# Performance work log

Hardware: AMD Instinct MI355X
Metric: run time of the kernel (lower is better)

## Reference

```python
import jax, jax.numpy as jnp
import numpy as np

D_MODEL = 768
D_STATE = 16
D_CONV = 4
EXPAND = 2
D_INNER = D_MODEL * EXPAND
B, L = 2, 2048


def _silu(x):
    return x * jax.nn.sigmoid(x)


def _ssm_core(xn, inw, cw, cb, xw, dtw, dtb, Alog, Dp, outw):
    """Mamba selective SSM. xn: [B,L,d_model] -> [B,L,d_model]."""
    Bn, Ln, _ = xn.shape
    S = Alog.shape[1]
    d_inner = Alog.shape[0]
    k = cw.shape[-1]
    xz = xn @ inw                      # [B,L,2*d_inner]
    xi, z = jnp.split(xz, 2, axis=-1)
    # depthwise causal conv along L (torch pads both sides then slices [:L] == left-pad k-1)
    xc = jnp.swapaxes(xi, 1, 2)        # [B,d_inner,L]
    xc = jax.lax.conv_general_dilated(xc, cw, (1,), [(k - 1, 0)],
                                      feature_group_count=d_inner)
    xc = xc + cb[None, :, None]
    xc = _silu(jnp.swapaxes(xc, 1, 2))  # [B,L,d_inner]
    bcdt = xc @ xw                     # [B,L,1+2S]
    dt_raw = bcdt[..., :1]
    Bs = bcdt[..., 1:1 + S]            # [B,L,S]
    Cs = bcdt[..., 1 + S:]             # [B,L,S]
    dt = jax.nn.softplus(dt_raw * dtw[None, None, :] + dtb)  # [B,L,d_inner]
    A = -jnp.exp(jnp.clip(Alog, -6.0, 6.0))                  # [d_inner,S]
    dA = jnp.exp(dt[..., None] * A[None, None])               # [B,L,d_inner,S]
    dBx = dt[..., None] * Bs[:, :, None, :] * xc[..., None]   # [B,L,d_inner,S]

    def step(h, ins):
        dA_t, dBx_t, C_t = ins
        h = jnp.clip(dA_t * h + dBx_t, -10000.0, 10000.0)
        return h, jnp.einsum('bds,bs->bd', h, C_t)

    h0 = jnp.zeros((Bn, d_inner, S), xc.dtype)
    _, ys = jax.lax.scan(step, h0, (jnp.moveaxis(dA, 1, 0),
                                    jnp.moveaxis(dBx, 1, 0),
                                    jnp.moveaxis(Cs, 1, 0)))
    y = jnp.moveaxis(ys, 0, 1) + xc * Dp[None, None]
    y = y * _silu(z)
    return y @ outw


def setup_inputs() -> dict:
    key = jax.random.key(0)
    ks = jax.random.split(key, 20)
    def core_params(koff):
        return dict(
            inw=jax.random.normal(ks[koff + 0], (D_MODEL, 2 * D_INNER), jnp.float32) * 0.02,
            cw=jax.random.normal(ks[koff + 1], (D_INNER, 1, D_CONV), jnp.float32) * 0.2,
            cb=jnp.zeros((D_INNER,), jnp.float32),
            xw=jax.random.normal(ks[koff + 2], (D_INNER, 1 + 2 * D_STATE), jnp.float32) * 0.02,
            dtw=jax.random.normal(ks[koff + 3], (D_INNER,), jnp.float32) * 0.5,
            dtb=jax.random.normal(ks[koff + 4], (D_INNER,), jnp.float32) * 0.1,
            Alog=jnp.clip(jnp.log(jnp.arange(1, D_STATE + 1, dtype=jnp.float32))[None, :]
                          * jnp.ones((D_INNER, 1), jnp.float32), -6.0, 6.0),
            D=jnp.ones((D_INNER,), jnp.float32),
            outw=jax.random.normal(ks[koff + 5], (D_INNER, D_MODEL), jnp.float32) * 0.02,
        )
    f = core_params(2)
    b = core_params(8)
    return {
        'x': jax.random.normal(ks[0], (B, L, D_MODEL), jnp.float32),
        'ln_g': jnp.ones((D_MODEL,), jnp.float32),
        'ln_b': jnp.zeros((D_MODEL,), jnp.float32),
        'alpha': jnp.zeros((), jnp.float32),
        'f_inw': f['inw'], 'f_cw': f['cw'], 'f_cb': f['cb'], 'f_xw': f['xw'],
        'f_dtw': f['dtw'], 'f_dtb': f['dtb'], 'f_Alog': f['Alog'], 'f_D': f['D'], 'f_outw': f['outw'],
        'b_inw': b['inw'], 'b_cw': b['cw'], 'b_cb': b['cb'], 'b_xw': b['xw'],
        'b_dtw': b['dtw'], 'b_dtb': b['dtb'], 'b_Alog': b['Alog'], 'b_D': b['D'], 'b_outw': b['outw'],
    }


def reference(x, ln_g, ln_b, alpha,
              f_inw, f_cw, f_cb, f_xw, f_dtw, f_dtb, f_Alog, f_D, f_outw,
              b_inw, b_cw, b_cb, b_xw, b_dtw, b_dtb, b_Alog, b_D, b_outw):
    residual = x.astype(jnp.float32)
    mu = residual.mean(-1, keepdims=True)
    var = ((residual - mu) ** 2).mean(-1, keepdims=True)
    xn = (residual - mu) / jnp.sqrt(var + 1e-5) * ln_g + ln_b
    y_fwd = _ssm_core(xn, f_inw, f_cw, f_cb, f_xw, f_dtw, f_dtb, f_Alog, f_D, f_outw)
    y_bwd = jnp.flip(_ssm_core(jnp.flip(xn, 1), b_inw, b_cw, b_cb, b_xw,
                               b_dtw, b_dtb, b_Alog, b_D, b_outw), 1)
    a = jax.nn.sigmoid(alpha)
    y = a * y_fwd + (1.0 - a) * y_bwd
    return y + residual
```

## Files before the change

kernel.cpp:

```cpp
#include <hip/hip_runtime.h>
#include <cstddef>
#include <cstdint>

#define DMODEL 768
#define DINNER 1536
#define NSTATE 16
#define LSEQ   2048
#define NB     2
#define NTOK   (NB*LSEQ)
#define NBCDT  33

#define TC     32
#define NCHUNK (LSEQ/TC)
#define KSPLIT 12
#define LOG2E  1.44269504f

typedef __bf16 bf16x8 __attribute__((ext_vector_type(8)));
typedef float  floatx4 __attribute__((ext_vector_type(4)));
typedef unsigned short us8 __attribute__((ext_vector_type(8)));

__device__ __forceinline__ float exp2_hw(float x) { return __builtin_amdgcn_exp2f(x); }
__device__ __forceinline__ float silu_f(float x) { return x / (1.f + expf(-x)); }
__device__ __forceinline__ float clip1e4(float x) {
    return __builtin_amdgcn_fmed3f(x, -1e4f, 1e4f);
}
__device__ __forceinline__ unsigned short f2bf(float f) {
    unsigned int u = __float_as_uint(f);
    unsigned int r = u + 0x7fffu + ((u >> 16) & 1u);
    return (unsigned short)(r >> 16);
}
__device__ __forceinline__ float bf2f(unsigned short u) {
    return __uint_as_float((unsigned int)u << 16);
}
__device__ __forceinline__ unsigned int pack2bf(float a, float b) {
    unsigned int ua = __float_as_uint(a); ua = ua + 0x7fffu + ((ua >> 16) & 1u);
    unsigned int ub = __float_as_uint(b); ub = ub + 0x7fffu + ((ub >> 16) & 1u);
    return (ua >> 16) | (ub & 0xffff0000u);
}
__device__ __forceinline__ void ld_lds16(unsigned short* lds, const unsigned short* g) {
    __builtin_amdgcn_global_load_lds(
        (const __attribute__((address_space(1))) unsigned int*)g,
        (__attribute__((address_space(3))) unsigned int*)lds,
        16, 0, 0);
}

__global__ void ln_kernel(const float* __restrict__ x,
                          const float* __restrict__ g,
                          const float* __restrict__ be,
                          unsigned short* __restrict__ xnb,
                          float* __restrict__ bcdt) {
    int row = blockIdx.x;
    int tid = threadIdx.x;
    int zi = row * 256 + tid;
    if (zi < 2 * NTOK * NBCDT) bcdt[zi] = 0.f;
    const float* xr = x + (size_t)row * DMODEL;
    float s = 0.f, ss = 0.f;
    for (int i = tid; i < DMODEL; i += 256) {
        float v = xr[i];
        s += v; ss += v * v;
    }
    for (int o = 32; o >= 1; o >>= 1) {
        s  += __shfl_xor(s,  o, 64);
        ss += __shfl_xor(ss, o, 64);
    }
    __shared__ float sS[4], sSS[4];
    int w = tid >> 6;
    if ((tid & 63) == 0) { sS[w] = s; sSS[w] = ss; }
    __syncthreads();
    s  = sS[0] + sS[1] + sS[2] + sS[3];
    ss = sSS[0] + sSS[1] + sSS[2] + sSS[3];
    float mu = s / DMODEL;
    float var = ss / DMODEL - mu * mu;
    float rstd = rsqrtf(var + 1e-5f);
    unsigned short* xo = xnb + (size_t)row * DMODEL;
    for (int i = tid; i < DMODEL; i += 256)
        xo[i] = f2bf((xr[i] - mu) * rstd * g[i] + be[i]);
}

__global__ __launch_bounds__(256)
void cast_weights(const float* __restrict__ f_inw, const float* __restrict__ b_inw,
                  const float* __restrict__ f_outw, const float* __restrict__ b_outw,
                  const float* __restrict__ f_xw, const float* __restrict__ b_xw,
                  const float* __restrict__ alpha,
                  unsigned short* __restrict__ inwT, unsigned short* __restrict__ outwT,
                  unsigned short* __restrict__ xwT) {
    __shared__ float t[32][33];
    int bid = blockIdx.x;
    int tid = threadIdx.x;
    int lr = tid >> 5, lc = tid & 31;
    if (bid < 4608) {
        int n0 = (bid % 192) * 32;
        int k0 = (bid / 192) * 32;
        const float* w = (n0 >= 3072) ? b_inw : f_inw;
        int nb = (n0 >= 3072) ? (n0 - 3072) : n0;
        #pragma unroll
        for (int r = 0; r < 4; r++)
            t[r * 8 + lr][lc] = w[(size_t)(k0 + r * 8 + lr) * 3072 + nb + lc];
        __syncthreads();
        #pragma unroll
        for (int r = 0; r < 4; r++)
            inwT[(size_t)(n0 + r * 8 + lr) * DMODEL + k0 + lc] = f2bf(t[lc][r * 8 + lr]);
    } else if (bid < 6912) {
        bid -= 4608;
        float a = 1.f / (1.f + expf(-alpha[0]));
        int n0 = (bid % 24) * 32;
        int k0 = (bid / 24) * 32;
        const float* w = (k0 >= DINNER) ? b_outw : f_outw;
        float sc = (k0 >= DINNER) ? (1.f - a) : a;
        int kb = (k0 >= DINNER) ? (k0 - DINNER) : k0;
        #pragma unroll
        for (int r = 0; r < 4; r++)
            t[r * 8 + lr][lc] = w[(size_t)(kb + r * 8 + lr) * DMODEL + n0 + lc];
        __syncthreads();
        #pragma unroll
        for (int r = 0; r < 4; r++)
            outwT[(size_t)(n0 + r * 8 + lr) * 3072 + k0 + lc] = f2bf(sc * t[lc][r * 8 + lr]);
    } else {
        bid -= 6912;
        int dir = bid / 48;
        int k0 = (bid % 48) * 32;
        const float* xw = dir ? b_xw : f_xw;
        unsigned short* dst = xwT + (size_t)dir * 48 * DINNER;
        for (int idx = tid; idx < 48 * 32; idx += 256) {
            int n = idx >> 5, kk = idx & 31;
            float v = (n < 33) ? xw[(size_t)(k0 + kk) * 33 + n] : 0.f;
            dst[(size_t)n * DINNER + k0 + kk] = f2bf(v);
        }
    }
}

__global__ __launch_bounds__(256)
void gemm_xz_mfma(const unsigned short* __restrict__ xnb,
                  const unsigned short* __restrict__ inwT,
                  unsigned short* __restrict__ xi, unsigned short* __restrict__ sz) {
    __shared__ unsigned short SH[128 * 136];
    unsigned short* Asm = SH;
    unsigned short* Bsm = SH + 128 * 64;
    int tid = threadIdx.x;
    int bm = blockIdx.y * 128;
    int bn = blockIdx.x * 128;
    int wave = tid >> 6, lane = tid & 63;
    int wm = (wave & 1) * 64, wn = (wave >> 1) * 64;
    int col15 = lane & 15, quad = lane >> 4;
    int lrow = lane >> 3;
    int lk   = (((lane & 7) ^ lrow) * 8);
    floatx4 acc[4][4];
    #pragma unroll
    for (int i = 0; i < 4; i++)
        #pragma unroll
        for (int j = 0; j < 4; j++)
            acc[i][j] = (floatx4){0.f, 0.f, 0.f, 0.f};

    int sw = col15 & 7;
    for (int k0 = 0; k0 < DMODEL; k0 += 64) {
        #pragma unroll
        for (int i = 0; i < 4; i++) {
            int r8 = wave * 32 + i * 8;
            int ra = r8 + lrow;
            ld_lds16(&Asm[r8 * 64], &xnb[(size_t)(bm + ra) * DMODEL + k0 + lk]);
            ld_lds16(&Bsm[r8 * 64], &inwT[(size_t)(bn + ra) * DMODEL + k0 + lk]);
        }
        __syncthreads();
        #pragma unroll
        for (int k2 = 0; k2 < 2; k2++) {
            bf16x8 af[4], bf_[4];
            int pc = ((k2 * 4 + quad) ^ sw) * 8;
            #pragma unroll
            for (int mt = 0; mt < 4; mt++)
                af[mt] = *(const bf16x8*)(&Asm[(wm + mt * 16 + col15) * 64 + pc]);
            #pragma unroll
            for (int nt = 0; nt < 4; nt++)
                bf_[nt] = *(const bf16x8*)(&Bsm[(wn + nt * 16 + col15) * 64 + pc]);
            #pragma unroll
            for (int mt = 0; mt < 4; mt++)
                #pragma unroll
                for (int nt = 0; nt < 4; nt++)
                    acc[mt][nt] = __builtin_amdgcn_mfma_f32_16x16x32_bf16(
                        af[mt], bf_[nt], acc[mt][nt], 0, 0, 0);
        }
        __syncthreads();
    }
    int dirq = (bn >= 3072) ? 1 : 0;
    int cb0  = bn - dirq * 3072;
    int zs   = (cb0 >= DINNER) ? 1 : 0;
    int ccb  = cb0 - zs * DINNER;
    unsigned short* dst = zs ? sz : xi;
    unsigned short* C16 = SH;
    #pragma unroll
    for (int mt = 0; mt < 4; mt++)
        #pragma unroll
        for (int nt = 0; nt < 4; nt++)
            #pragma unroll
            for (int r = 0; r < 4; r++) {
                int row = wm + mt * 16 + quad * 4 + r;
                int col = wn + nt * 16 + col15;
                float v = acc[mt][nt][r];
                if (zs) v = silu_f(v);
                C16[row * 136 + col] = f2bf(v);
            }
    __syncthreads();
    {
        int erow = tid >> 4;
        int cch  = tid & 15;
        size_t rowbase = (size_t)dirq * NTOK + bm;
        #pragma unroll
        for (int p = 0; p < 8; p++) {
            int row = p * 16 + erow;
            uint4 v = *(const uint4*)(&C16[row * 136 + cch * 8]);
            *(uint4*)(&dst[(rowbase + row) * DINNER + ccb + cch * 8]) = v;
        }
    }
}

__global__ __launch_bounds__(256)
void bcdt_conv_gemm_mfma(const unsigned short* __restrict__ xi,
                         const float* __restrict__ f_cw, const float* __restrict__ f_cb,
                         const float* __restrict__ b_cw, const float* __restrict__ b_cb,
                         const unsigned short* __restrict__ xwT,
                         float* __restrict__ bcdt) {
    __shared__ unsigned short Xs[131 * 64];
    __shared__ unsigned short As[128 * 64];
    __shared__ unsigned short Bs[48 * 64];
    int tid = threadIdx.x;
    int wave = tid >> 6, lane = tid & 63;
    int r0 = blockIdx.x * 128;
    int kc = blockIdx.y;
    int dirb = r0 >> 11;
    int dir = dirb >> 1, b = dirb & 1;
    int u0 = r0 & 2047;
    const float* cw = dir ? b_cw : f_cw;
    const float* cb = dir ? b_cb : f_cb;
    size_t xibase = ((size_t)dir * NTOK + (size_t)b * LSEQ) * DINNER;
    const unsigned short* Bsrc = xwT + (size_t)dir * 48 * DINNER;

    int col15 = lane & 15, quad = lane >> 4;
    int sw = col15 & 7;
    int lrow = lane >> 3;
    int lcc = (lane & 7) * 8;
    int lk  = (((lane & 7) ^ lrow) * 8);
    int wm = wave * 32;

    int cp = (tid & 31) * 2;
    int rg = (tid >> 5) * 16;

    floatx4 acc[2][3];
    #pragma unroll
    for (int i = 0; i < 2; i++)
        #pragma unroll
        for (int j = 0; j < 3; j++)
            acc[i][j] = (floatx4){0.f, 0.f, 0.f, 0.f};

    for (int ks = 0; ks < 2; ks++) {
        int kb = kc * 128 + ks * 64;
        #pragma unroll
        for (int i = 0; i < 2; i++) {
            int g = wave + i * 4;
            if (g < 6)
                ld_lds16(&Bs[g * 8 * 64],
                         &Bsrc[(size_t)(g * 8 + lrow) * DINNER + kb + lk]);
        }
        #pragma unroll
        for (int i = 0; i < 4; i++) {
            int g = wave * 4 + i;
            int u = u0 + g * 8 + lrow;
            int l = dir ? (LSEQ - 1 - u) : u;
            ld_lds16(&Xs[(3 + g * 8) * 64], &xi[xibase + (size_t)l * DINNER + kb + lcc]);
        }
        if (tid < 96) {
            int hh = tid >> 5, c2 = (tid & 31) * 2;
            int u = u0 - 3 + hh;
            unsigned int v = 0;
            if (u >= 0) {
                int l = dir ? (LSEQ - 1 - u) : u;
                v = *(const unsigned int*)(&xi[xibase + (size_t)l * DINNER + kb + c2]);
            }
            *(unsigned int*)(&Xs[hh * 64 + c2]) = v;
        }
        __syncthreads();
        {
            int ch0 = kb + cp;
            float4 w0 = *(const float4*)(cw + (size_t)ch0 * 4);
            float4 w1 = *(const float4*)(cw + (size_t)(ch0 + 1) * 4);
            float cb0 = cb[ch0], cb1 = cb[ch0 + 1];
            unsigned int v;
            v = *(const unsigned int*)(&Xs[(rg + 0) * 64 + cp]);
            float a3 = bf2f((unsigned short)v), b3 = bf2f((unsigned short)(v >> 16));
            v = *(const unsigned int*)(&Xs[(rg + 1) * 64 + cp]);
            float a2 = bf2f((unsigned short)v), b2 = bf2f((unsigned short)(v >> 16));
            v = *(const unsigned int*)(&Xs[(rg + 2) * 64 + cp]);
            float a1 = bf2f((unsigned short)v), b1 = bf2f((unsigned short)(v >> 16));
            int cs = cp >> 3, e = cp & 7;
            #pragma unroll
            for (int j = 0; j < 16; j++) {
                int r = rg + j;
                v = *(const unsigned int*)(&Xs[(r + 3) * 64 + cp]);
                float a0 = bf2f((unsigned short)v), b0 = bf2f((unsigned short)(v >> 16));
                float xa = cb0;
                xa = fmaf(w0.x, a3, xa); xa = fmaf(w0.y, a2, xa);
                xa = fmaf(w0.z, a1, xa); xa = fmaf(w0.w, a0, xa);
                xa = silu_f(xa);
                float xb = cb1;
                xb = fmaf(w1.x, b3, xb); xb = fmaf(w1.y, b2, xb);
                xb = fmaf(w1.z, b1, xb); xb = fmaf(w1.w, b0, xb);
                xb = silu_f(xb);
                a3 = a2; a2 = a1; a1 = a0;
                b3 = b2; b2 = b1; b1 = b0;
                int ad = r * 64 + ((cs ^ (r & 7)) << 3) + e;
                *(unsigned int*)(&As[ad]) = pack2bf(xa, xb);
            }
        }
        __syncthreads();
        #pragma unroll
        for (int k2 = 0; k2 < 2; k2++) {
            int pc = ((k2 * 4 + quad) ^ sw) * 8;
            bf16x8 af[2], bfr[3];
            #pragma unroll
            for (int mt = 0; mt < 2; mt++)
                af[mt] = *(const bf16x8*)(&As[(wm + mt * 16 + col15) * 64 + pc]);
            #pragma unroll
            for (int nt = 0; nt < 3; nt++)
                bfr[nt] = *(const bf16x8*)(&Bs[(nt * 16 + col15) * 64 + pc]);
            #pragma unroll
            for (int mt = 0; mt < 2; mt++)
                #pragma unroll
                for (int nt = 0; nt < 3; nt++)
                    acc[mt][nt] = __builtin_amdgcn_mfma_f32_16x16x32_bf16(
                        af[mt], bfr[nt], acc[mt][nt], 0, 0, 0);
        }
        __syncthreads();
    }
    #pragma unroll
    for (int mt = 0; mt < 2; mt++) {
        #pragma unroll
        for (int nt = 0; nt < 3; nt++) {
            int n = nt * 16 + col15;
            if (n < 33) {
                #pragma unroll
                for (int r = 0; r < 4; r++) {
                    int row = r0 + wm + mt * 16 + quad * 4 + r;
                    atomicAdd(&bcdt[(size_t)row * 33 + n], acc[mt][nt][r]);
                }
            }
        }
    }
}

__global__ __launch_bounds__(256)
void scan_p1(const unsigned short* __restrict__ xi, const float* __restrict__ bcdt,
             const float* __restrict__ f_cw, const float* __restrict__ f_cb,
             const float* __restrict__ b_cw, const float* __restrict__ b_cb,
             const float* __restrict__ f_dtw, const float* __restrict__ f_dtb,
             const float* __restrict__ f_Alog,
             const float* __restrict__ b_dtw, const float* __restrict__ b_dtb,
             const float* __restrict__ b_Alog,
             float* __restrict__ Sdtbuf, float* __restrict__ hloc) {
    int tid = threadIdx.x;
    int d = blockIdx.x * 256 + tid;
    int chunk = blockIdx.y;
    int dirb  = blockIdx.z;
    int dir = dirb >> 1, b = dirb & 1;
    const float* dtw  = dir ? b_dtw  : f_dtw;
    const float* dtb  = dir ? b_dtb  : f_dtb;
    const float* Alog = dir ? b_Alog : f_Alog;
    const float* cw   = dir ? b_cw   : f_cw;
    const float* cb   = dir ? b_cb   : f_cb;
    float dtw_d = dtw[d], dtb_d = dtb[d];
    float4 wc = *(const float4*)(cw + (size_t)d * 4);
    float cb_d = cb[d];
    float A2[NSTATE], h[NSTATE];
    #pragma unroll
    for (int s = 0; s < NSTATE; s++) {
        float al = fminf(fmaxf(Alog[d * NSTATE + s], -6.f), 6.f);
        A2[s] = -__expf(al) * LOG2E;
        h[s] = 0.f;
    }
    float Sdt = 0.f;
    int t0 = chunk * TC;
    size_t xbase = ((size_t)dir * NTOK + (size_t)b * LSEQ) * DINNER + d;
    long stride = dir ? -(long)DINNER : (long)DINNER;
    int l0 = dir ? (LSEQ - 1 - t0) : t0;
    const unsigned short* xp = xi + xbase + (size_t)l0 * DINNER;
    float xm3 = 0.f, xm2 = 0.f, xm1 = 0.f;
    if (chunk) {
        xm3 = bf2f(*(xp - 3 * stride));
        xm2 = bf2f(*(xp - 2 * stride));
        xm1 = bf2f(*(xp - 1 * stride));
    }
    size_t rbase = (size_t)dirb * LSEQ + (size_t)t0;
    const float* bc = bcdt + rbase * NBCDT;
    for (int t = 0; t < TC; t++) {
        float cur = bf2f(*xp); xp += stride;
        float xv = cb_d;
        xv = fmaf(wc.x, xm3, xv);
        xv = fmaf(wc.y, xm2, xv);
        xv = fmaf(wc.z, xm1, xv);
        xv = fmaf(wc.w, cur, xv);
        xv = silu_f(xv);
        xm3 = xm2; xm2 = xm1; xm1 = cur;
        float dt_raw = bc[t * NBCDT];
        float u = fmaf(dt_raw, dtw_d, dtb_d);
        float dt = fmaxf(u, 0.f) + __logf(1.f + __expf(-fabsf(u)));
        Sdt += dt;
        float dtx = dt * xv;
        #pragma unroll
        for (int s = 0; s < NSTATE; s++) {
            float Bv = bc[t * NBCDT + 1 + s];
            h[s] = fmaf(exp2_hw(dt * A2[s]), h[s], dtx * Bv);
        }
    }
    Sdtbuf[(size_t)chunk * (4 * DINNER) + (size_t)dirb * DINNER + d] = Sdt;
    size_t base = ((size_t)chunk * 4 + dirb) * ((size_t)DINNER * NSTATE) + (size_t)d * NSTATE;
    #pragma unroll
    for (int s = 0; s < NSTATE; s++)
        hloc[base + s] = h[s];
}

__global__ void scan_p2(const float* __restrict__ Sdtbuf, const float* __restrict__ hloc,
                        const float* __restrict__ f_Alog, const float* __restrict__ b_Alog,
                        float* __restrict__ hin) {
    int i = blockIdx.x * 256 + threadIdx.x;
    const int DS = DINNER * NSTATE;
    int dirb = i / DS;
    int rem = i - dirb * DS;
    int d = rem >> 4, s = rem & 15;
    const float* Alog = (dirb >> 1) ? b_Alog : f_Alog;
    float al = fminf(fmaxf(Alog[d * NSTATE + s], -6.f), 6.f);
    float A2 = -__expf(al) * LOG2E;
    float h = 0.f;
    const int stride = 4 * DS;
    const int sstr = 4 * DINNER;
    for (int c = 0; c < NCHUNK; c++) {
        size_t idx = (size_t)c * stride + i;
        hin[idx] = h;
        float P = exp2_hw(A2 * Sdtbuf[(size_t)c * sstr + dirb * DINNER + d]);
        h = clip1e4(fmaf(P, h, hloc[idx]));
    }
}

__global__ __launch_bounds__(256)
void scan_p3(const unsigned short* __restrict__ xi, const float* __restrict__ bcdt,
             const unsigned short* __restrict__ sz, const float* __restrict__ hin,
             const float* __restrict__ f_cw, const float* __restrict__ f_cb,
             const float* __restrict__ b_cw, const float* __restrict__ b_cb,
             const float* __restrict__ f_dtw, const float* __restrict__ f_dtb,
             const float* __restrict__ f_Alog, const float* __restrict__ f_D,
             const float* __restrict__ b_dtw, const float* __restrict__ b_dtb,
             const float* __restrict__ b_Alog, const float* __restrict__ b_D,
             unsigned short* __restrict__ yvb) {
    int tid = threadIdx.x;
    int d = blockIdx.x * 256 + tid;
    int chunk = blockIdx.y;
    int dirb  = blockIdx.z;
    int dir = dirb >> 1, b = dirb & 1;
    const float* dtw  = dir ? b_dtw  : f_dtw;
    const float* dtb  = dir ? b_dtb  : f_dtb;
    const float* Alog = dir ? b_Alog : f_Alog;
    const float* Dp   = dir ? b_D    : f_D;
    const float* cw   = dir ? b_cw   : f_cw;
    const float* cb   = dir ? b_cb   : f_cb;
    float dtw_d = dtw[d], dtb_d = dtb[d], D_d = Dp[d];
    float4 wc = *(const float4*)(cw + (size_t)d * 4);
    float cb_d = cb[d];
    float A2[NSTATE], h[NSTATE];
    size_t hbase = ((size_t)chunk * 4 + dirb) * ((size_t)DINNER * NSTATE) + (size_t)d * NSTATE;
    #pragma unroll
    for (int s = 0; s < NSTATE; s++) {
        float al = fminf(fmaxf(Alog[d * NSTATE + s], -6.f), 6.f);
        A2[s] = -__expf(al) * LOG2E;
        h[s] = hin[hbase + s];
    }
    int t0 = chunk * TC;
    size_t xbase = ((size_t)dir * NTOK + (size_t)b * LSEQ) * DINNER + d;
    long stride = dir ? -(long)DINNER : (long)DINNER;
    int l0 = dir ? (LSEQ - 1 - t0) : t0;
    const unsigned short* xp = xi + xbase + (size_t)l0 * DINNER;
    const unsigned short* szp = sz + xbase + (size_t)l0 * DINNER;
    unsigned short* yp = yvb + ((size_t)(b * LSEQ + l0)) * 3072 + dir * DINNER + d;
    long ystride = stride * 2;
    float xm3 = 0.f, xm2 = 0.f, xm1 = 0.f;
    if (chunk) {
        xm3 = bf2f(*(xp - 3 * stride));
        xm2 = bf2f(*(xp - 2 * stride));
        xm1 = bf2f(*(xp - 1 * stride));
    }
    size_t rbase = (size_t)dirb * LSEQ + (size_t)t0;
    const float* bc = bcdt + rbase * NBCDT;
    for (int t = 0; t < TC; t++) {
        float cur = bf2f(*xp); xp += stride;
        float xv = cb_d;
        xv = fmaf(wc.x, xm3, xv);
        xv = fmaf(wc.y, xm2, xv);
        xv = fmaf(wc.z, xm1, xv);
        xv = fmaf(wc.w, cur, xv);
        xv = silu_f(xv);
        xm3 = xm2; xm2 = xm1; xm1 = cur;
        float dt_raw = bc[t * NBCDT];
        float u = fmaf(dt_raw, dtw_d, dtb_d);
        float dt = fmaxf(u, 0.f) + __logf(1.f + __expf(-fabsf(u)));
        float dtx = dt * xv;
        float p = 0.f;
        #pragma unroll
        for (int s = 0; s < NSTATE; s++) {
            float Bv = bc[t * NBCDT + 1 + s];
            float Cv = bc[t * NBCDT + 1 + NSTATE + s];
            h[s] = fmaf(exp2_hw(dt * A2[s]), h[s], dtx * Bv);
            p = fmaf(h[s], Cv, p);
        }
        float szv = bf2f(*szp); szp += stride;
        float y = (p + xv * D_d) * szv;
        *yp = f2bf(y); yp += ystride;
    }
}

__global__ __launch_bounds__(256)
void gemm_out_mfma(const unsigned short* __restrict__ yvb,
                   const unsigned short* __restrict__ outwT,
                   const float* __restrict__ x,
                   float* __restrict__ out) {
    __shared__ unsigned short Asm[128 * 64];
    __shared__ unsigned short Bsm[64 * 64];
    int tid = threadIdx.x;
    int bm = blockIdx.y * 128;
    int bn = blockIdx.x * 64;
    int wave = tid >> 6, lane = tid & 63;
    int wm = (wave & 1) * 64, wn = (wave >> 1) * 32;
    int col15 = lane & 15, quad = lane >> 4;
    int lrow = lane >> 3;
    int lk   = (((lane & 7) ^ lrow) * 8);
    floatx4 acc[4][2];
    #pragma unroll
    for (int i = 0; i < 4; i++)
        #pragma unroll
        for (int j = 0; j < 2; j++)
            acc[i][j] = (floatx4){0.f, 0.f, 0.f, 0.f};

    int sw = col15 & 7;
    for (int k0 = 0; k0 < 2 * DINNER; k0 += 64) {
        #pragma unroll
        for (int i = 0; i < 4; i++) {
            int r8 = wave * 32 + i * 8;
            ld_lds16(&Asm[r8 * 64], &yvb[(size_t)(bm + r8 + lrow) * 3072 + k0 + lk]);
        }
        #pragma unroll
        for (int i = 0; i < 2; i++) {
            int r8 = wave * 16 + i * 8;
            ld_lds16(&Bsm[r8 * 64], &outwT[(size_t)(bn + r8 + lrow) * 3072 + k0 + lk]);
        }
        __syncthreads();
        #pragma unroll
        for (int k2 = 0; k2 < 2; k2++) {
            bf16x8 af[4], bf_[2];
            int pc = ((k2 * 4 + quad) ^ sw) * 8;
            #pragma unroll
            for (int mt = 0; mt < 4; mt++)
                af[mt] = *(const bf16x8*)(&Asm[(wm + mt * 16 + col15) * 64 + pc]);
            #pragma unroll
            for (int nt = 0; nt < 2; nt++)
                bf_[nt] = *(const bf16x8*)(&Bsm[(wn + nt * 16 + col15) * 64 + pc]);
            #pragma unroll
            for (int mt = 0; mt < 4; mt++)
                #pragma unroll
                for (int nt = 0; nt < 2; nt++)
                    acc[mt][nt] = __builtin_amdgcn_mfma_f32_16x16x32_bf16(
                        af[mt], bf_[nt], acc[mt][nt], 0, 0, 0);
        }
        __syncthreads();
    }
    #pragma unroll
    for (int mt = 0; mt < 4; mt++) {
        #pragma unroll
        for (int nt = 0; nt < 2; nt++) {
            #pragma unroll
            for (int r = 0; r < 4; r++) {
                int row = bm + wm + mt * 16 + quad * 4 + r;
                int gn  = bn + wn + nt * 16 + col15;
                out[(size_t)row * DMODEL + gn] = acc[mt][nt][r] + x[(size_t)row * DMODEL + gn];
            }
        }
    }
}

extern "C" void kernel_launch(void* const* d_in, const int* in_sizes, int n_in,
                              void* d_out, int out_size, void* d_ws, size_t ws_size,
                              hipStream_t stream) {
    const float* x     = (const float*)d_in[0];
    const float* ln_g  = (const float*)d_in[1];
    const float* ln_b  = (const float*)d_in[2];
    const float* alpha = (const float*)d_in[3];
    const float* f_inw  = (const float*)d_in[4];
    const float* f_cw   = (const float*)d_in[5];
    const float* f_cb   = (const float*)d_in[6];
    const float* f_xw   = (const float*)d_in[7];
    const float* f_dtw  = (const float*)d_in[8];
    const float* f_dtb  = (const float*)d_in[9];
    const float* f_Alog = (const float*)d_in[10];
    const float* f_D    = (const float*)d_in[11];
    const float* f_outw = (const float*)d_in[12];
    const float* b_inw  = (const float*)d_in[13];
    const float* b_cw   = (const float*)d_in[14];
    const float* b_cb   = (const float*)d_in[15];
    const float* b_xw   = (const float*)d_in[16];
    const float* b_dtw  = (const float*)d_in[17];
    const float* b_dtb  = (const float*)d_in[18];
    const float* b_Alog = (const float*)d_in[19];
    const float* b_D    = (const float*)d_in[20];
    const float* b_outw = (const float*)d_in[21];
    float* out = (float*)d_out;

    float* ws = (float*)d_ws;
    float* r_xnb  = ws;
    float* r_inwT = r_xnb + 1572864;
    float* r_outwT= r_inwT + 2359296;
    float* r_xib  = r_outwT + 1179648;
    float* r_szb  = r_xib + 6291456;
    float* r_yvb  = r_szb + 6291456;
    float* hloc   = r_yvb + 6291456;
    float* hin    = hloc + 6291456;
    float* Sdtbuf = hin + 6291456;
    float* bcdt   = Sdtbuf + 393216;

    unsigned short* xnb   = (unsigned short*)r_xnb;
    unsigned short* inwT  = (unsigned short*)r_inwT;
    unsigned short* outwT = (unsigned short*)r_outwT;
    unsigned short* xib   = (unsigned short*)r_xib;
    unsigned short* szb   = (unsigned short*)r_szb;
    unsigned short* yvb   = (unsigned short*)r_yvb;
    unsigned short* xwT   = (unsigned short*)hloc;

    ln_kernel<<<NTOK, 256, 0, stream>>>(x, ln_g, ln_b, xnb, bcdt);
    cast_weights<<<4608 + 2304 + 96, 256, 0, stream>>>(f_inw, b_inw, f_outw, b_outw,
                                                       f_xw, b_xw, alpha,
                                                       inwT, outwT, xwT);
    {
        dim3 grid(6144 / 128, NTOK / 128);
        gemm_xz_mfma<<<grid, 256, 0, stream>>>(xnb, inwT, xib, szb);
    }
    {
        dim3 g(2 * NTOK / 128, KSPLIT);
        bcdt_conv_gemm_mfma<<<g, 256, 0, stream>>>(xib, f_cw, f_cb, b_cw, b_cb,
                                                   xwT, bcdt);
    }
    {
        dim3 grid1(DINNER / 256, NCHUNK, 4);
        scan_p1<<<grid1, 256, 0, stream>>>(xib, bcdt, f_cw, f_cb, b_cw, b_cb,
                                           f_dtw, f_dtb, f_Alog,
                                           b_dtw, b_dtb, b_Alog, Sdtbuf, hloc);
        scan_p2<<<(4 * DINNER * NSTATE) / 256, 256, 0, stream>>>(Sdtbuf, hloc,
                                                                 f_Alog, b_Alog, hin);
        scan_p3<<<grid1, 256, 0, stream>>>(xib, bcdt, szb, hin,
                                           f_cw, f_cb, b_cw, b_cb,
                                           f_dtw, f_dtb, f_Alog, f_D,
                                           b_dtw, b_dtb, b_Alog, b_D, yvb);
    }
    {
        dim3 grid(DMODEL / 64, NTOK / 128);
        gemm_out_mfma<<<grid, 256, 0, stream>>>(yvb, outwT, x, out);
    }
}
```

Baseline: 393.9 us.

## Double-buffer GEMM LDS tiles and split-K the output GEMM with atomics

Both the input-projection GEMM and the output GEMM now use two LDS buffers, so the next K tile is fetched while the current one goes through MFMA. The output GEMM is split into two K halves over a third grid dimension, and each half atomically adds its partial sum into the output. The layernorm kernel pre-writes the residual into the output so those atomics accumulate onto it. The aim is to hide global-load latency and give the small output GEMM more blocks; the cost is doubled LDS use, which may lower occupancy, plus atomic traffic and a summation order that is not deterministic.

```diff
diff --git a/kernel.cpp b/kernel.cpp
--- a/kernel.cpp
+++ b/kernel.cpp
@@ -17,7 +17,6 @@
 
 typedef __bf16 bf16x8 __attribute__((ext_vector_type(8)));
 typedef float  floatx4 __attribute__((ext_vector_type(4)));
-typedef unsigned short us8 __attribute__((ext_vector_type(8)));
 
 __device__ __forceinline__ float exp2_hw(float x) { return __builtin_amdgcn_exp2f(x); }
 __device__ __forceinline__ float silu_f(float x) { return x / (1.f + expf(-x)); }
@@ -48,7 +47,8 @@
                           const float* __restrict__ g,
                           const float* __restrict__ be,
                           unsigned short* __restrict__ xnb,
-                          float* __restrict__ bcdt) {
+                          float* __restrict__ bcdt,
+                          float* __restrict__ out) {
     int row = blockIdx.x;
     int tid = threadIdx.x;
     int zi = row * 256 + tid;
@@ -73,8 +73,12 @@
     float var = ss / DMODEL - mu * mu;
     float rstd = rsqrtf(var + 1e-5f);
     unsigned short* xo = xnb + (size_t)row * DMODEL;
-    for (int i = tid; i < DMODEL; i += 256)
-        xo[i] = f2bf((xr[i] - mu) * rstd * g[i] + be[i]);
+    float* ores = out + (size_t)row * DMODEL;
+    for (int i = tid; i < DMODEL; i += 256) {
+        float v = xr[i];
+        xo[i] = f2bf((v - mu) * rstd * g[i] + be[i]);
+        ores[i] = v;
+    }
 }
 
 __global__ __launch_bounds__(256)
@@ -133,9 +137,7 @@
 void gemm_xz_mfma(const unsigned short* __restrict__ xnb,
                   const unsigned short* __restrict__ inwT,
                   unsigned short* __restrict__ xi, unsigned short* __restrict__ sz) {
-    __shared__ unsigned short SH[128 * 136];
-    unsigned short* Asm = SH;
-    unsigned short* Bsm = SH + 128 * 64;
+    __shared__ unsigned short SH[2][2 * 128 * 64];
     int tid = threadIdx.x;
     int bm = blockIdx.y * 128;
     int bn = blockIdx.x * 128;
@@ -152,25 +154,37 @@
             acc[i][j] = (floatx4){0.f, 0.f, 0.f, 0.f};
 
     int sw = col15 & 7;
-    for (int k0 = 0; k0 < DMODEL; k0 += 64) {
-        #pragma unroll
-        for (int i = 0; i < 4; i++) {
-            int r8 = wave * 32 + i * 8;
-            int ra = r8 + lrow;
-            ld_lds16(&Asm[r8 * 64], &xnb[(size_t)(bm + ra) * DMODEL + k0 + lk]);
-            ld_lds16(&Bsm[r8 * 64], &inwT[(size_t)(bn + ra) * DMODEL + k0 + lk]);
-        }
-        __syncthreads();
+
+#define STAGE_XZ(buf, k0)                                                       \
+    {                                                                           \
+        unsigned short* Abuf = SH[buf];                                         \
+        unsigned short* Bbuf = SH[buf] + 128 * 64;                              \
+        _Pragma("unroll")                                                       \
+        for (int i = 0; i < 4; i++) {                                           \
+            int r8 = wave * 32 + i * 8;                                         \
+            int ra = r8 + lrow;                                                 \
+            ld_lds16(&Abuf[r8 * 64], &xnb[(size_t)(bm + ra) * DMODEL + (k0) + lk]); \
+            ld_lds16(&Bbuf[r8 * 64], &inwT[(size_t)(bn + ra) * DMODEL + (k0) + lk]); \
+        }                                                                       \
+    }
+
+    STAGE_XZ(0, 0);
+    __syncthreads();
+    int cur = 0;
+    for (int kt = 0; kt < DMODEL / 64; ++kt) {
+        if (kt + 1 < DMODEL / 64) STAGE_XZ(cur ^ 1, (kt + 1) * 64);
+        const unsigned short* Acur = SH[cur];
+        const unsigned short* Bcur = SH[cur] + 128 * 64;
         #pragma unroll
         for (int k2 = 0; k2 < 2; k2++) {
             bf16x8 af[4], bf_[4];
             int pc = ((k2 * 4 + quad) ^ sw) * 8;
             #pragma unroll
             for (int mt = 0; mt < 4; mt++)
-                af[mt] = *(const bf16x8*)(&Asm[(wm + mt * 16 + col15) * 64 + pc]);
+                af[mt] = *(const bf16x8*)(&Acur[(wm + mt * 16 + col15) * 64 + pc]);
             #pragma unroll
             for (int nt = 0; nt < 4; nt++)
-                bf_[nt] = *(const bf16x8*)(&Bsm[(wn + nt * 16 + col15) * 64 + pc]);
+                bf_[nt] = *(const bf16x8*)(&Bcur[(wn + nt * 16 + col15) * 64 + pc]);
             #pragma unroll
             for (int mt = 0; mt < 4; mt++)
                 #pragma unroll
@@ -179,13 +193,14 @@
                         af[mt], bf_[nt], acc[mt][nt], 0, 0, 0);
         }
         __syncthreads();
+        cur ^= 1;
     }
     int dirq = (bn >= 3072) ? 1 : 0;
     int cb0  = bn - dirq * 3072;
     int zs   = (cb0 >= DINNER) ? 1 : 0;
     int ccb  = cb0 - zs * DINNER;
     unsigned short* dst = zs ? sz : xi;
-    unsigned short* C16 = SH;
+    unsigned short* C16 = &SH[0][0];
     #pragma unroll
     for (int mt = 0; mt < 4; mt++)
         #pragma unroll
@@ -210,6 +225,7 @@
             *(uint4*)(&dst[(rowbase + row) * DINNER + ccb + cch * 8]) = v;
         }
     }
+#undef STAGE_XZ
 }
 
 __global__ __launch_bounds__(256)
@@ -515,13 +531,12 @@
 __global__ __launch_bounds__(256)
 void gemm_out_mfma(const unsigned short* __restrict__ yvb,
                    const unsigned short* __restrict__ outwT,
-                   const float* __restrict__ x,
                    float* __restrict__ out) {
-    __shared__ unsigned short Asm[128 * 64];
-    __shared__ unsigned short Bsm[64 * 64];
+    __shared__ unsigned short SH[2][(128 + 64) * 64];
     int tid = threadIdx.x;
     int bm = blockIdx.y * 128;
     int bn = blockIdx.x * 64;
+    int ks = blockIdx.z;
     int wave = tid >> 6, lane = tid & 63;
     int wm = (wave & 1) * 64, wn = (wave >> 1) * 32;
     int col15 = lane & 15, quad = lane >> 4;
@@ -535,28 +550,41 @@
             acc[i][j] = (floatx4){0.f, 0.f, 0.f, 0.f};
 
     int sw = col15 & 7;
-    for (int k0 = 0; k0 < 2 * DINNER; k0 += 64) {
-        #pragma unroll
-        for (int i = 0; i < 4; i++) {
-            int r8 = wave * 32 + i * 8;
-            ld_lds16(&Asm[r8 * 64], &yvb[(size_t)(bm + r8 + lrow) * 3072 + k0 + lk]);
-        }
-        #pragma unroll
-        for (int i = 0; i < 2; i++) {
-            int r8 = wave * 16 + i * 8;
-            ld_lds16(&Bsm[r8 * 64], &outwT[(size_t)(bn + r8 + lrow) * 3072 + k0 + lk]);
-        }
-        __syncthreads();
+    int kbase = ks * DINNER;
+
+#define STAGE_OUT(buf, k0)                                                      \
+    {                                                                           \
+        unsigned short* Abuf = SH[buf];                                         \
+        unsigned short* Bbuf = SH[buf] + 128 * 64;                              \
+        _Pragma("unroll")                                                       \
+        for (int i = 0; i < 4; i++) {                                           \
+            int r8 = wave * 32 + i * 8;                                         \
+            ld_lds16(&Abuf[r8 * 64], &yvb[(size_t)(bm + r8 + lrow) * 3072 + (k0) + lk]); \
+        }                                                                       \
+        _Pragma("unroll")                                                       \
+        for (int i = 0; i < 2; i++) {                                           \
+            int r8 = wave * 16 + i * 8;                                         \
+            ld_lds16(&Bbuf[r8 * 64], &outwT[(size_t)(bn + r8 + lrow) * 3072 + (k0) + lk]); \
+        }                                                                       \
+    }
+
+    STAGE_OUT(0, kbase);
+    __syncthreads();
+    int cur = 0;
+    for (int kt = 0; kt < DINNER / 64; ++kt) {
+        if (kt + 1 < DINNER / 64) STAGE_OUT(cur ^ 1, kbase + (kt + 1) * 64);
+        const unsigned short* Acur = SH[cur];
+        const unsigned short* Bcur = SH[cur] + 128 * 64;
         #pragma unroll
         for (int k2 = 0; k2 < 2; k2++) {
             bf16x8 af[4], bf_[2];
             int pc = ((k2 * 4 + quad) ^ sw) * 8;
             #pragma unroll
             for (int mt = 0; mt < 4; mt++)
-                af[mt] = *(const bf16x8*)(&Asm[(wm + mt * 16 + col15) * 64 + pc]);
+                af[mt] = *(const bf16x8*)(&Acur[(wm + mt * 16 + col15) * 64 + pc]);
             #pragma unroll
             for (int nt = 0; nt < 2; nt++)
-                bf_[nt] = *(const bf16x8*)(&Bsm[(wn + nt * 16 + col15) * 64 + pc]);
+                bf_[nt] = *(const bf16x8*)(&Bcur[(wn + nt * 16 + col15) * 64 + pc]);
             #pragma unroll
             for (int mt = 0; mt < 4; mt++)
                 #pragma unroll
@@ -565,6 +593,7 @@
                         af[mt], bf_[nt], acc[mt][nt], 0, 0, 0);
         }
         __syncthreads();
+        cur ^= 1;
     }
     #pragma unroll
     for (int mt = 0; mt < 4; mt++) {
@@ -574,10 +603,11 @@
             for (int r = 0; r < 4; r++) {
                 int row = bm + wm + mt * 16 + quad * 4 + r;
                 int gn  = bn + wn + nt * 16 + col15;
-                out[(size_t)row * DMODEL + gn] = acc[mt][nt][r] + x[(size_t)row * DMODEL + gn];
+                atomicAdd(&out[(size_t)row * DMODEL + gn], acc[mt][nt][r]);
             }
         }
     }
+#undef STAGE_OUT
 }
 
 extern "C" void kernel_launch(void* const* d_in, const int* in_sizes, int n_in,
@@ -627,7 +657,7 @@
     unsigned short* yvb   = (unsigned short*)r_yvb;
     unsigned short* xwT   = (unsigned short*)hloc;
 
-    ln_kernel<<<NTOK, 256, 0, stream>>>(x, ln_g, ln_b, xnb, bcdt);
+    ln_kernel<<<NTOK, 256, 0, stream>>>(x, ln_g, ln_b, xnb, bcdt, out);
     cast_weights<<<4608 + 2304 + 96, 256, 0, stream>>>(f_inw, b_inw, f_outw, b_outw,
                                                        f_xw, b_xw, alpha,
                                                        inwT, outwT, xwT);
@@ -653,7 +683,7 @@
                                            b_dtw, b_dtb, b_Alog, b_D, yvb);
     }
     {
-        dim3 grid(DMODEL / 64, NTOK / 128);
-        gemm_out_mfma<<<grid, 256, 0, stream>>>(yvb, outwT, x, out);
-    }
-}
+        dim3 grid(DMODEL / 64, NTOK / 128, 2);
+        gemm_out_mfma<<<grid, 256, 0, stream>>>(yvb, outwT, out);
+    }
+}
```

Result: no change. 398.3 us (+1.1%).
